# Optimization experiments

Hardware: AMD Instinct MI355X
Metric: run time of the kernel (lower is better)

## Reference

```python
import jax, jax.numpy as jnp
import numpy as np

N_BASES = 4  # a,c,g,u
L = 4096


def setup_inputs() -> dict:
    key = jax.random.key(0)
    seq_ids = jax.random.randint(key, (L,), 0, N_BASES, dtype=jnp.int64)
    # BASE_DICT: each base -> one-hot vector of length N_BASES (identity table)
    base_table = jnp.eye(N_BASES, dtype=jnp.float32)
    return {"seq_ids": seq_ids, "base_table": base_table}


def reference(seq_ids, base_table):
    # one_hot[i] = BASE_DICT[sequence[i]]  -> (L, N_BASES)
    one_hot = base_table[seq_ids]
    n = one_hot.shape[0]
    # ret[:, i, j] = cat(one_hot[i], one_hot[j])
    row = jnp.broadcast_to(one_hot[:, None, :], (n, n, N_BASES))  # first half, varies with i
    col = jnp.broadcast_to(one_hot[None, :, :], (n, n, N_BASES))  # second half, varies with j
    ret = jnp.concatenate([row, col], axis=-1)        # (L, L, 2*N_BASES)
    ret = jnp.transpose(ret, (2, 0, 1))               # (2*N_BASES, L, L)
    return ret[None]                                  # (1, 2*N_BASES, L, L)
```

## Files before the change

kernel.cpp:

```cpp
#include <hip/hip_runtime.h>
#include <hip/hip_bf16.h>


#define L 4096
#define TOTAL_F4 (8u * L * L / 4u)

typedef float v4f __attribute__((ext_vector_type(4)));
typedef int   v4i __attribute__((ext_vector_type(4)));

__global__ __launch_bounds__(256) void SequenceEmbedding_30923764532139_kernel(
        const int* __restrict__ seq,
        const float* __restrict__ table,
        v4f* __restrict__ out) {
    unsigned idx = blockIdx.x * blockDim.x + threadIdx.x;
    unsigned e = idx << 2;
    unsigned c = e >> 24;
    unsigned i = (e >> 12) & (L - 1);
    unsigned j = e & (L - 1);

    v4f val;
    if (c < 4u) {
        float x = table[(unsigned)seq[i] * 4u + c];
        val = (v4f){x, x, x, x};
    } else {
        unsigned cc = c - 4u;
        v4i s = *(const v4i*)(seq + j);
        val.x = table[(unsigned)s.x * 4u + cc];
        val.y = table[(unsigned)s.y * 4u + cc];
        val.z = table[(unsigned)s.z * 4u + cc];
        val.w = table[(unsigned)s.w * 4u + cc];
    }
    __builtin_nontemporal_store(val, out + idx);
}

extern "C" void kernel_launch(void* const* d_in, const int* in_sizes, int n_in,
                              void* d_out, int out_size, void* d_ws, size_t ws_size,
                              hipStream_t stream) {
    const int*   seq   = (const int*)d_in[0];
    const float* table = (const float*)d_in[1];
    v4f*         out   = (v4f*)d_out;

    dim3 block(256);
    dim3 grid(TOTAL_F4 / 256u);
    SequenceEmbedding_30923764532139_kernel<<<grid, block, 0, stream>>>(seq, table, out);
}
```

Before: 510.9 us.

## Give each block four full rows per plane and reuse loaded column values

Each block now writes four full output rows of one channel plane (16 float4 stores per thread) instead of one float4 per thread, so the grid drops from 131072 blocks to 8192. Column-half values are computed once per thread and reused across the four rows. Table lookups become selects between four preloaded table entries instead of dependent gathers. The aim is to cut per-element index math and load overhead in a store-bound kernel, at the cost of fewer, longer-running blocks.

```diff
diff --git a/kernel.cpp b/kernel.cpp
--- a/kernel.cpp
+++ b/kernel.cpp
@@ -3,7 +3,6 @@
 
 
 #define L 4096
-#define TOTAL_F4 (8u * L * L / 4u)
 
 typedef float v4f __attribute__((ext_vector_type(4)));
 typedef int   v4i __attribute__((ext_vector_type(4)));
@@ -11,26 +10,55 @@
 __global__ __launch_bounds__(256) void SequenceEmbedding_30923764532139_kernel(
         const int* __restrict__ seq,
         const float* __restrict__ table,
-        v4f* __restrict__ out) {
-    unsigned idx = blockIdx.x * blockDim.x + threadIdx.x;
-    unsigned e = idx << 2;
-    unsigned c = e >> 24;
-    unsigned i = (e >> 12) & (L - 1);
-    unsigned j = e & (L - 1);
+        float* __restrict__ out) {
+    unsigned b = blockIdx.x;
+    unsigned t = threadIdx.x;
+    unsigned c = b >> 10;
+    unsigned g = b & 1023u;
+    unsigned i0 = g << 2;
+    unsigned cc = c & 3u;
 
-    v4f val;
+    float t0 = table[0u * 4u + cc];
+    float t1 = table[1u * 4u + cc];
+    float t2 = table[2u * 4u + cc];
+    float t3 = table[3u * 4u + cc];
+
+    size_t plane = (size_t)c << 24;
+    v4f* outv = (v4f*)out;
+
     if (c < 4u) {
-        float x = table[(unsigned)seq[i] * 4u + c];
-        val = (v4f){x, x, x, x};
+        #pragma unroll
+        for (int r = 0; r < 4; ++r) {
+            unsigned i = i0 + (unsigned)r;
+            int s = seq[i];
+            float x = s == 0 ? t0 : s == 1 ? t1 : s == 2 ? t2 : t3;
+            v4f val = {x, x, x, x};
+            size_t base = (plane + (size_t)i * L) >> 2;
+            #pragma unroll
+            for (int k = 0; k < 4; ++k)
+                __builtin_nontemporal_store(val, outv + base + t + 256u * (unsigned)k);
+        }
     } else {
-        unsigned cc = c - 4u;
-        v4i s = *(const v4i*)(seq + j);
-        val.x = table[(unsigned)s.x * 4u + cc];
-        val.y = table[(unsigned)s.y * 4u + cc];
-        val.z = table[(unsigned)s.z * 4u + cc];
-        val.w = table[(unsigned)s.w * 4u + cc];
+        v4f vals[4];
+        #pragma unroll
+        for (int k = 0; k < 4; ++k) {
+            unsigned jf4 = t + 256u * (unsigned)k;
+            v4i s = *(const v4i*)(seq + 4u * jf4);
+            v4f v;
+            v.x = s.x == 0 ? t0 : s.x == 1 ? t1 : s.x == 2 ? t2 : t3;
+            v.y = s.y == 0 ? t0 : s.y == 1 ? t1 : s.y == 2 ? t2 : t3;
+            v.z = s.z == 0 ? t0 : s.z == 1 ? t1 : s.z == 2 ? t2 : t3;
+            v.w = s.w == 0 ? t0 : s.w == 1 ? t1 : s.w == 2 ? t2 : t3;
+            vals[k] = v;
+        }
+        #pragma unroll
+        for (int r = 0; r < 4; ++r) {
+            size_t base = (plane + (size_t)(i0 + (unsigned)r) * L) >> 2;
+            #pragma unroll
+            for (int k = 0; k < 4; ++k)
+                __builtin_nontemporal_store(vals[k], outv + base + t + 256u * (unsigned)k);
+        }
     }
-    __builtin_nontemporal_store(val, out + idx);
 }
 
 extern "C" void kernel_launch(void* const* d_in, const int* in_sizes, int n_in,
@@ -38,9 +66,9 @@
                               hipStream_t stream) {
     const int*   seq   = (const int*)d_in[0];
     const float* table = (const float*)d_in[1];
-    v4f*         out   = (v4f*)d_out;
+    float*       out   = (float*)d_out;
 
     dim3 block(256);
-    dim3 grid(TOTAL_F4 / 256u);
+    dim3 grid(8192);
     SequenceEmbedding_30923764532139_kernel<<<grid, block, 0, stream>>>(seq, table, out);
 }
```

Result: slower. 528.0 us (+3.4%).

## Use persistent grid-stride threads with register-cached lookup table

Applied to the files above, without the earlier changes.

Launches a fixed grid of 2048 blocks in which each thread loops over 64 float4 outputs, instead of one thread per float4. The 16-entry table is loaded into registers once per thread, and the nontemporal store is replaced by a plain store. This aims to cut per-thread launch and indexing overhead and repeated table loads. The risks are dynamic indexing into the register array, which may spill to scratch, and the loss of the nontemporal hint on a store-bound kernel.

```diff
diff --git a/kernel.cpp b/kernel.cpp
--- a/kernel.cpp
+++ b/kernel.cpp
@@ -3,7 +3,9 @@
 
 
 #define L 4096
+#define NTHREADS (2048u * 256u)
 #define TOTAL_F4 (8u * L * L / 4u)
+#define NITER (TOTAL_F4 / NTHREADS)
 
 typedef float v4f __attribute__((ext_vector_type(4)));
 typedef int   v4i __attribute__((ext_vector_type(4)));
@@ -12,25 +14,37 @@
         const int* __restrict__ seq,
         const float* __restrict__ table,
         v4f* __restrict__ out) {
-    unsigned idx = blockIdx.x * blockDim.x + threadIdx.x;
-    unsigned e = idx << 2;
-    unsigned c = e >> 24;
-    unsigned i = (e >> 12) & (L - 1);
-    unsigned j = e & (L - 1);
+    unsigned tid = blockIdx.x * blockDim.x + threadIdx.x;
 
-    v4f val;
-    if (c < 4u) {
-        float x = table[(unsigned)seq[i] * 4u + c];
-        val = (v4f){x, x, x, x};
-    } else {
-        unsigned cc = c - 4u;
-        v4i s = *(const v4i*)(seq + j);
-        val.x = table[(unsigned)s.x * 4u + cc];
-        val.y = table[(unsigned)s.y * 4u + cc];
-        val.z = table[(unsigned)s.z * 4u + cc];
-        val.w = table[(unsigned)s.w * 4u + cc];
+    float tab[16];
+    #pragma unroll
+    for (int q = 0; q < 4; ++q) {
+        v4f r = *(const v4f*)(table + 4 * q);
+        tab[4 * q + 0] = r.x; tab[4 * q + 1] = r.y;
+        tab[4 * q + 2] = r.z; tab[4 * q + 3] = r.w;
     }
-    __builtin_nontemporal_store(val, out + idx);
+
+    #pragma unroll
+    for (unsigned k = 0; k < NITER; ++k) {
+        unsigned idx = tid + k * NTHREADS;
+        unsigned c   = idx >> 22;
+        unsigned i   = (idx >> 10) & (L - 1);
+        unsigned jf4 = idx & 1023u;
+        unsigned cc  = c & 3u;
+
+        v4f val;
+        if (c < 4u) {
+            float x = tab[4u * (unsigned)seq[i] + cc];
+            val = (v4f){x, x, x, x};
+        } else {
+            v4i s = *(const v4i*)(seq + 4u * jf4);
+            val.x = tab[4u * (unsigned)s.x + cc];
+            val.y = tab[4u * (unsigned)s.y + cc];
+            val.z = tab[4u * (unsigned)s.z + cc];
+            val.w = tab[4u * (unsigned)s.w + cc];
+        }
+        out[idx] = val;
+    }
 }
 
 extern "C" void kernel_launch(void* const* d_in, const int* in_sizes, int n_in,
@@ -40,7 +54,6 @@
     const float* table = (const float*)d_in[1];
     v4f*         out   = (v4f*)d_out;
 
-    dim3 block(256);
-    dim3 grid(TOTAL_F4 / 256u);
-    SequenceEmbedding_30923764532139_kernel<<<grid, block, 0, stream>>>(seq, table, out);
+    SequenceEmbedding_30923764532139_kernel<<<dim3(2048), dim3(256), 0, stream>>>(
+        seq, table, out);
 }
```

After: 524.8 us. 1.03x slower.
